# Kernel tuning notes

Hardware: AMD Instinct MI355X
Metric: run time of the kernel (lower is better)

## Reference

```python
import jax, jax.numpy as jnp
import numpy as np

NUM_TOKENS = 8192
DIM = 256
BETA = 0.25
DECAY = 0.99
EPS = 1e-05


def setup_inputs() -> dict:
    key = jax.random.key(0)
    k1, k2 = jax.random.split(key, 2)
    z = jax.random.normal(k1, (16, DIM, 32, 32), dtype=jnp.float32)
    embedding = jax.random.normal(k2, (NUM_TOKENS, DIM), dtype=jnp.float32)
    cluster_size = jnp.zeros((NUM_TOKENS,), dtype=jnp.float32)
    ema_w = embedding  # module init copies embed_init into both embedding and ema_w
    return {"z": z, "embedding": embedding, "cluster_size": cluster_size, "ema_w": ema_w}


def reference(z, embedding, cluster_size, ema_w):
    # z: [B, D, H, W] -> [B, H, W, D]
    zp = jnp.transpose(z, (0, 2, 3, 1))
    zf = zp.reshape(-1, DIM)  # [N, D]
    # squared euclidean distances [N, K] via ||z||^2 + ||e||^2 - 2 z.e
    d = (jnp.sum(zf * zf, axis=1, keepdims=True)
         + jnp.sum(embedding * embedding, axis=1)
         - 2.0 * (zf @ embedding.T))
    idx = jnp.argmin(d, axis=1)  # [N]
    z_q = embedding[idx].reshape(zp.shape)  # [B, H, W, D]

    # training-mode EMA statistics (pure-functional: returned as new states)
    counts = jax.ops.segment_sum(jnp.ones(zf.shape[0], dtype=zf.dtype), idx,
                                 num_segments=NUM_TOKENS)
    embed_sum = jax.ops.segment_sum(zf, idx, num_segments=NUM_TOKENS)  # [K, D]
    cs = cluster_size * DECAY + (1.0 - DECAY) * counts
    new_ema_w = ema_w * DECAY + (1.0 - DECAY) * embed_sum
    # torch evaluates sum AFTER add_(eps): denom = sum(cs + eps) + K*eps
    cs = cs + EPS
    new_cluster_size = cs / (jnp.sum(cs) + NUM_TOKENS * EPS)
    new_embedding = new_ema_w / new_cluster_size[:, None]

    loss = BETA * jnp.mean((jax.lax.stop_gradient(z_q) - zp) ** 2)
    # straight-through estimator
    z_q_st = zp + jax.lax.stop_gradient(z_q - zp)
    out = jnp.transpose(z_q_st, (0, 3, 1, 2))  # back to [B, D, H, W]
    return out, loss, idx, new_cluster_size, new_ema_w, new_embedding
```

## Files before the change

### kernel.cpp

```cpp
#include <hip/hip_runtime.h>

#define N_TOK   16384
#define K_CODES 8192
#define DIMS    256

#define OUT_OFF  0
#define LOSS_OFF 4194304
#define IDX_OFF  4194305
#define NCS_OFF  4210689
#define NEMA_OFF 4218881
#define NEMB_OFF 6316033

#define WS_ZFRAG  0u
#define WS_EFRAG  16777216u
#define WS_ENORM  25165824u
#define WS_PVAL   25198592u
#define WS_PIDX   25460736u
#define WS_IDXI   25722880u
#define WS_CNT    25788416u
#define WS_CS     25821184u
#define WS_OFFS   25853952u
#define WS_WPOS   25886720u
#define WS_TLIST  25919488u
#define WS_DENOM  25985024u

typedef _Float16 f16x8 __attribute__((ext_vector_type(8)));
typedef float    f32x16 __attribute__((ext_vector_type(16)));

union HU { _Float16 h; unsigned short u; };

static __device__ inline void split_f32(float x, unsigned short& hi, unsigned short& lo) {
    HU a; a.h = (_Float16)x;
    float r = (x - (float)a.h) * 2048.0f;
    HU b; b.h = (_Float16)r;
    hi = a.u; lo = b.u;
}

static __device__ inline float join_f16(unsigned short h, unsigned short l) {
    HU a, b; a.u = h; b.u = l;
    return (float)a.h + (float)b.h * 4.8828125e-4f;
}

#define GLD16(gp, lp) __builtin_amdgcn_global_load_lds( \
    (const __attribute__((address_space(1))) unsigned int*)(gp), \
    (__attribute__((address_space(3))) unsigned int*)(lp), 16, 0, 0)

__global__ __launch_bounds__(256) void cvt_z_kernel(const float* __restrict__ z,
                                                    unsigned short* __restrict__ zfrag,
                                                    float* __restrict__ loss_cell,
                                                    double* __restrict__ denom) {
    __shared__ float T[64][65];
    const int t = threadIdx.x;
    const int hg = blockIdx.x & 15, dg = (blockIdx.x >> 4) & 3, b = blockIdx.x >> 6;
    if (blockIdx.x == 0 && t == 0) { *loss_cell = 0.f; *denom = 0.0; }
    const int c4 = (t & 15) * 4, r0 = t >> 4;
    const float* zb = z + (((size_t)(b * 256 + dg * 64)) << 10) + hg * 64;
#pragma unroll
    for (int p = 0; p < 4; ++p) {
        const int r = r0 + p * 16;
        const float4 v = *(const float4*)(zb + ((size_t)r << 10) + c4);
        T[r][c4] = v.x; T[r][c4 + 1] = v.y; T[r][c4 + 2] = v.z; T[r][c4 + 3] = v.w;
    }
    __syncthreads();
    const int tr = t & 63, dc = (t >> 6) * 16;
    const int tile = b * 16 + hg;
    const int tg = tile * 2 + (tr >> 5), l31 = tr & 31;
    const int ks = dg * 4 + (dc >> 4);
    unsigned short hb[16], lb[16];
#pragma unroll
    for (int j = 0; j < 16; ++j) split_f32(T[dc + j][tr], hb[j], lb[j]);
#pragma unroll
    for (int lv = 0; lv < 2; ++lv) {
        const unsigned short* src = lv ? lb : hb;
        unsigned short* dst = zfrag + (size_t)((tg * 2 + lv) * 16 + ks) * 512;
        *(uint4*)(dst + l31 * 8)       = ((const uint4*)src)[0];
        *(uint4*)(dst + 256 + l31 * 8) = ((const uint4*)src)[1];
    }
}

__global__ __launch_bounds__(256) void cvt_e_enorm(const float* __restrict__ emb,
                                                   unsigned short* __restrict__ efrag,
                                                   float* __restrict__ enorm,
                                                   int* __restrict__ cnt) {
    __shared__ double red[256];
    const int t = threadIdx.x, g = blockIdx.x;
    const int lane = t & 63, q = t >> 6;
    const int l31 = lane & 31, lhi = lane >> 5;
    if (g < 32) cnt[g * 256 + t] = 0;
    const float* rowp = emb + (size_t)(g * 32 + l31) * 256 + lhi * 8;
    double s = 0.0;
#pragma unroll
    for (int kk = 0; kk < 4; ++kk) {
        const int ks = q * 4 + kk;
        const float4 a = *(const float4*)(rowp + ks * 16);
        const float4 bq = *(const float4*)(rowp + ks * 16 + 4);
        const float vv[8] = {a.x, a.y, a.z, a.w, bq.x, bq.y, bq.z, bq.w};
        unsigned short hb[8], lb[8];
#pragma unroll
        for (int j = 0; j < 8; ++j) {
            split_f32(vv[j], hb[j], lb[j]);
            s += (double)vv[j] * (double)vv[j];
        }
        *(uint4*)(efrag + (size_t)((g * 2 + 0) * 16 + ks) * 512 + lane * 8) = *(const uint4*)hb;
        *(uint4*)(efrag + (size_t)((g * 2 + 1) * 16 + ks) * 512 + lane * 8) = *(const uint4*)lb;
    }
    red[t] = s;
    __syncthreads();
    if (t < 32) {
        double acc = 0.0;
#pragma unroll
        for (int qq = 0; qq < 4; ++qq) acc += red[qq * 64 + t] + red[qq * 64 + 32 + t];
        enorm[g * 32 + t] = (float)acc;
    }
}

__global__ __launch_bounds__(256, 2) void argmin_mfma(
    const unsigned short* __restrict__ zfrag, const unsigned short* __restrict__ efrag,
    const float* __restrict__ enorm, float* __restrict__ pval, int* __restrict__ pidx) {
    __shared__ __align__(16) unsigned short E[2][8192];
    __shared__ float en_s[2][64];

    const int tid = threadIdx.x, lane = tid & 63, wave = tid >> 6;
    const int tile = blockIdx.x & 127, csplit = blockIdx.x >> 7;
    const int token0 = tile * 128, code0 = csplit * 2048;

    f16x8 Zr[2][16];
    {
        const unsigned short* zb = zfrag + (size_t)(tile * 4 + wave) * 16384 + lane * 8;
#pragma unroll
        for (int lv = 0; lv < 2; ++lv)
#pragma unroll
            for (int ks = 0; ks < 16; ++ks)
                Zr[lv][ks] = *(const f16x8*)(zb + (lv * 16 + ks) * 512);
    }

    const int slv = wave >> 1, scg = wave & 1;

    float bv = 3.4e38f; int bi = 0;

#pragma unroll
    for (int ksl = 0; ksl < 4; ++ksl) {
        const unsigned short* sp = efrag +
            (size_t)(((csplit * 64 + scg) * 2 + slv) * 16 + ksl) * 512 + lane * 8;
        GLD16(sp, &E[0][(wave * 4 + ksl) * 512]);
    }
    if (tid < 64) en_s[0][tid] = enorm[code0 + tid];
    __syncthreads();

    for (int ct = 0; ct < 32; ++ct) {
        f32x16 acc_h[2], acc_l[2];
#pragma unroll
        for (int cg = 0; cg < 2; ++cg)
#pragma unroll
            for (int qq = 0; qq < 16; ++qq) { acc_h[cg][qq] = 0.f; acc_l[cg][qq] = 0.f; }

#pragma unroll
        for (int kc = 0; kc < 4; ++kc) {
            const int p = (ct * 4 + kc) & 1;
            if (!(ct == 31 && kc == 3)) {
                const int nch = ct * 4 + kc + 1;
                const int nct = nch >> 2, nkc = nch & 3;
                const int g = csplit * 64 + nct * 2 + scg;
#pragma unroll
                for (int ksl = 0; ksl < 4; ++ksl) {
                    const unsigned short* sp = efrag +
                        (size_t)((g * 2 + slv) * 16 + nkc * 4 + ksl) * 512 + lane * 8;
                    GLD16(sp, &E[p ^ 1][(wave * 4 + ksl) * 512]);
                }
            }
            if (kc == 0 && ct < 31 && tid < 64)
                en_s[(ct + 1) & 1][tid] = enorm[code0 + (ct + 1) * 64 + tid];

#pragma unroll
            for (int ksl = 0; ksl < 4; ++ksl) {
                const int ks = kc * 4 + ksl;
                f16x8 ae[2][2];
#pragma unroll
                for (int lv = 0; lv < 2; ++lv)
#pragma unroll
                    for (int cg = 0; cg < 2; ++cg)
                        ae[lv][cg] = *(const f16x8*)&E[p][((lv * 2 + cg) * 4 + ksl) * 512 + lane * 8];
#pragma unroll
                for (int cg = 0; cg < 2; ++cg) {
                    acc_h[cg] = __builtin_amdgcn_mfma_f32_32x32x16_f16(ae[0][cg], Zr[0][ks], acc_h[cg], 0, 0, 0);
                    acc_l[cg] = __builtin_amdgcn_mfma_f32_32x32x16_f16(ae[0][cg], Zr[1][ks], acc_l[cg], 0, 0, 0);
                    acc_l[cg] = __builtin_amdgcn_mfma_f32_32x32x16_f16(ae[1][cg], Zr[0][ks], acc_l[cg], 0, 0, 0);
                }
            }
            if (kc == 3) {
                const int rbase = 4 * (lane >> 5);
#pragma unroll
                for (int cg = 0; cg < 2; ++cg)
#pragma unroll
                    for (int r = 0; r < 16; ++r) {
                        const int cl = cg * 32 + (r & 3) + 8 * (r >> 2) + rbase;
                        const float s = en_s[ct & 1][cl] -
                            2.0f * (acc_h[cg][r] + acc_l[cg][r] * 4.8828125e-4f);
                        const int code = code0 + ct * 64 + cl;
                        if (s < bv) { bv = s; bi = code; }
                    }
            }
            __syncthreads();
        }
    }
    {
        const float ov = __shfl_xor(bv, 32);
        const int   oi = __shfl_xor(bi, 32);
        if (ov < bv || (ov == bv && oi < bi)) { bv = ov; bi = oi; }
    }
    if (lane < 32) {
        const int n = token0 + wave * 32 + lane;
        pval[csplit * N_TOK + n] = bv;
        pidx[csplit * N_TOK + n] = bi;
    }
}

__global__ __launch_bounds__(256) void combine4_kernel(
    const float* __restrict__ pval, const int* __restrict__ pidx,
    int* __restrict__ idx_i, float* __restrict__ idx_f, int* __restrict__ cnt) {
    const int n = blockIdx.x * 256 + threadIdx.x;
    float bv = pval[n]; int bi = pidx[n];
#pragma unroll
    for (int s = 1; s < 4; ++s) {
        const float v = pval[s * N_TOK + n];
        const int i = pidx[s * N_TOK + n];
        if (v < bv || (v == bv && i < bi)) { bv = v; bi = i; }
    }
    idx_i[n] = bi;
    idx_f[n] = (float)bi;
    atomicAdd(&cnt[bi], 1);
}

__global__ __launch_bounds__(256) void scan_kernel(const int* __restrict__ cnt,
                                                   int* __restrict__ offs,
                                                   int* __restrict__ wpos) {
    __shared__ int part[256];
    const int tid = threadIdx.x;
    const int base = tid * 32;
    int loc[32];
    int s = 0;
#pragma unroll
    for (int j = 0; j < 32; ++j) { loc[j] = cnt[base + j]; s += loc[j]; }
    part[tid] = s;
    __syncthreads();
    for (int off = 1; off < 256; off <<= 1) {
        int v = 0;
        if (tid >= off) v = part[tid - off];
        __syncthreads();
        if (tid >= off) part[tid] += v;
        __syncthreads();
    }
    int run = (tid > 0) ? part[tid - 1] : 0;
#pragma unroll
    for (int j = 0; j < 32; ++j) {
        offs[base + j] = run;
        wpos[base + j] = run;
        run += loc[j];
    }
}

__global__ __launch_bounds__(256) void scatter_cs(
    const int* __restrict__ idx_i, int* __restrict__ wpos, int* __restrict__ tlist,
    const float* __restrict__ cluster_size, const int* __restrict__ cnt,
    float* __restrict__ cs, double* __restrict__ denom) {
    __shared__ double red[256];
    const int t = threadIdx.x, b = blockIdx.x;
    if (b < 64) {
        const int n = b * 256 + t;
        const int k = idx_i[n];
        tlist[atomicAdd(&wpos[k], 1)] = n;
    } else {
        const int k = (b - 64) * 256 + t;
        const float v = cluster_size[k] * 0.99f + 0.01f * (float)cnt[k] + 1e-5f;
        cs[k] = v;
        red[t] = (double)v;
        __syncthreads();
        for (int s2 = 128; s2; s2 >>= 1) {
            if (t < s2) red[t] += red[t + s2];
            __syncthreads();
        }
        if (t == 0) atomicAdd(denom, red[0]);
    }
}

__global__ __launch_bounds__(256) void nema_gather(
    const unsigned short* __restrict__ zfrag,
    const int* __restrict__ offs, const int* __restrict__ cnt, const int* __restrict__ tlist,
    const float* __restrict__ ema_w, const float* __restrict__ cs,
    const double* __restrict__ denom, float* __restrict__ ncs_out,
    float* __restrict__ nema_out, float* __restrict__ nemb_out,
    const float* __restrict__ z, const float* __restrict__ emb,
    const int* __restrict__ idx_i, float* __restrict__ out, float* __restrict__ loss_cell) {
    __shared__ float redf[256];
    const int t = threadIdx.x;
    if (blockIdx.x < 2048) {
        const int lane = t & 63, wave = t >> 6;
        const int k = blockIdx.x * 4 + wave;
        const int l31 = lane & 31, sel = lane >> 5;
        const int beg = offs[k], c = cnt[k];
        float acc[8] = {0.f, 0.f, 0.f, 0.f, 0.f, 0.f, 0.f, 0.f};
        for (int i = 0; i < c; ++i) {
            const int tok = tlist[beg + i];
            const int tg = tok >> 5, tl = tok & 31;
            const uint4 v = *(const uint4*)(zfrag +
                (size_t)((tg * 2 + sel) * 16 + (l31 >> 1)) * 512 + (l31 & 1) * 256 + tl * 8);
            uint4 o;
            o.x = __shfl_xor((int)v.x, 32); o.y = __shfl_xor((int)v.y, 32);
            o.z = __shfl_xor((int)v.z, 32); o.w = __shfl_xor((int)v.w, 32);
            if (lane < 32) {
                const unsigned short* hp = (const unsigned short*)&v;
                const unsigned short* lp = (const unsigned short*)&o;
#pragma unroll
                for (int j = 0; j < 8; ++j) acc[j] += join_f16(hp[j], lp[j]);
            }
        }
        const float dn = (float)(*denom) + (float)K_CODES * 1e-5f;
        const float ncs = cs[k] / dn;
        if (lane == 0) ncs_out[k] = ncs;
        if (lane < 32) {
            const size_t off = ((size_t)k << 8) + l31 * 8;
#pragma unroll
            for (int j = 0; j < 8; ++j) {
                const float ne = ema_w[off + j] * 0.99f + 0.01f * acc[j];
                nema_out[off + j] = ne;
                nemb_out[off + j] = ne / ncs;
            }
        }
    } else {
        const int gb = blockIdx.x - 2048;
        const int n0 = (gb >> 2) * 64;
        const int dg = (gb & 3) * 64;
        const int b = n0 >> 10, hw0 = n0 & 1023;
        const int lane = t & 63, w = t >> 6;
        const int n = n0 + lane;
        const int k = idx_i[n];
        const float* zb = z + ((size_t)b << 18) + hw0 + lane;
        float* ob = out + ((size_t)b << 18) + hw0 + lane;
        float ls = 0.f;
#pragma unroll 4
        for (int d = dg + w; d < dg + 64; d += 4) {
            const float zv = zb[(size_t)d << 10];
            const float ev = emb[((size_t)k << 8) + d];
            ob[(size_t)d << 10] = ev;
            const float df = ev - zv;
            ls += df * df;
        }
        redf[t] = ls;
        __syncthreads();
        for (int s2 = 128; s2; s2 >>= 1) {
            if (t < s2) redf[t] += redf[t + s2];
            __syncthreads();
        }
        if (t == 0) atomicAdd(loss_cell, redf[0] * (0.25f / 4194304.0f));
    }
}

extern "C" void kernel_launch(void* const* d_in, const int* in_sizes, int n_in,
                              void* d_out, int out_size, void* d_ws, size_t ws_size,
                              hipStream_t stream) {
    const float* z            = (const float*)d_in[0];
    const float* emb          = (const float*)d_in[1];
    const float* cluster_size = (const float*)d_in[2];
    const float* ema_w        = (const float*)d_in[3];
    float* out = (float*)d_out;
    char*  wsb = (char*)d_ws;

    unsigned short* zfrag = (unsigned short*)(wsb + WS_ZFRAG);
    unsigned short* efrag = (unsigned short*)(wsb + WS_EFRAG);
    float*  enorm  = (float*)(wsb + WS_ENORM);
    float*  pval   = (float*)(wsb + WS_PVAL);
    int*    pidx   = (int*)(wsb + WS_PIDX);
    int*    idx_i  = (int*)(wsb + WS_IDXI);
    int*    cnt    = (int*)(wsb + WS_CNT);
    float*  cs     = (float*)(wsb + WS_CS);
    int*    offs   = (int*)(wsb + WS_OFFS);
    int*    wpos   = (int*)(wsb + WS_WPOS);
    int*    tlist  = (int*)(wsb + WS_TLIST);
    double* denom  = (double*)(wsb + WS_DENOM);

    cvt_z_kernel<<<1024, 256, 0, stream>>>(z, zfrag, out + LOSS_OFF, denom);
    cvt_e_enorm<<<256, 256, 0, stream>>>(emb, efrag, enorm, cnt);
    argmin_mfma<<<512, 256, 0, stream>>>(zfrag, efrag, enorm, pval, pidx);
    combine4_kernel<<<N_TOK / 256, 256, 0, stream>>>(pval, pidx, idx_i,
                                                     out + IDX_OFF, cnt);
    scan_kernel<<<1, 256, 0, stream>>>(cnt, offs, wpos);
    scatter_cs<<<96, 256, 0, stream>>>(idx_i, wpos, tlist, cluster_size, cnt, cs, denom);
    nema_gather<<<3072, 256, 0, stream>>>(zfrag, offs, cnt, tlist, ema_w, cs, denom,
                                          out + NCS_OFF, out + NEMA_OFF, out + NEMB_OFF,
                                          z, emb, idx_i, out + OUT_OFF, out + LOSS_OFF);
}
```

Measured before the change: 424.6 us.

## Fuse conversion kernels, use packed atomicMin argmin, reorder MFMAs, unroll gather

Merges the z and embedding conversion kernels into one launch, selected by block index. The per-split argmin partials are replaced with a packed 64-bit (order-preserving value, index) atomicMin, which turns the combine kernel into a plain extraction. The MFMA issue order is regrouped so that consecutive MFMAs do not depend on the same accumulator, and the nema gather loop is unrolled by two to keep more loads in flight. The main savings are launch overhead and partial-buffer traffic, paid for with atomics and an extra initialisation of the atomic buffer.

```diff
diff --git a/kernel.cpp b/kernel.cpp
--- a/kernel.cpp
+++ b/kernel.cpp
@@ -14,8 +14,7 @@
 #define WS_ZFRAG  0u
 #define WS_EFRAG  16777216u
 #define WS_ENORM  25165824u
-#define WS_PVAL   25198592u
-#define WS_PIDX   25460736u
+#define WS_AMIN   25198592u
 #define WS_IDXI   25722880u
 #define WS_CNT    25788416u
 #define WS_CS     25821184u
@@ -45,78 +44,78 @@
     (const __attribute__((address_space(1))) unsigned int*)(gp), \
     (__attribute__((address_space(3))) unsigned int*)(lp), 16, 0, 0)
 
-__global__ __launch_bounds__(256) void cvt_z_kernel(const float* __restrict__ z,
-                                                    unsigned short* __restrict__ zfrag,
-                                                    float* __restrict__ loss_cell,
-                                                    double* __restrict__ denom) {
-    __shared__ float T[64][65];
+__global__ __launch_bounds__(256) void fused_cvt(
+    const float* __restrict__ z, unsigned short* __restrict__ zfrag,
+    float* __restrict__ loss_cell, double* __restrict__ denom,
+    const float* __restrict__ emb, unsigned short* __restrict__ efrag,
+    float* __restrict__ enorm, int* __restrict__ cnt,
+    unsigned long long* __restrict__ amin) {
     const int t = threadIdx.x;
-    const int hg = blockIdx.x & 15, dg = (blockIdx.x >> 4) & 3, b = blockIdx.x >> 6;
-    if (blockIdx.x == 0 && t == 0) { *loss_cell = 0.f; *denom = 0.0; }
-    const int c4 = (t & 15) * 4, r0 = t >> 4;
-    const float* zb = z + (((size_t)(b * 256 + dg * 64)) << 10) + hg * 64;
-#pragma unroll
-    for (int p = 0; p < 4; ++p) {
-        const int r = r0 + p * 16;
-        const float4 v = *(const float4*)(zb + ((size_t)r << 10) + c4);
-        T[r][c4] = v.x; T[r][c4 + 1] = v.y; T[r][c4 + 2] = v.z; T[r][c4 + 3] = v.w;
-    }
-    __syncthreads();
-    const int tr = t & 63, dc = (t >> 6) * 16;
-    const int tile = b * 16 + hg;
-    const int tg = tile * 2 + (tr >> 5), l31 = tr & 31;
-    const int ks = dg * 4 + (dc >> 4);
-    unsigned short hb[16], lb[16];
-#pragma unroll
-    for (int j = 0; j < 16; ++j) split_f32(T[dc + j][tr], hb[j], lb[j]);
-#pragma unroll
-    for (int lv = 0; lv < 2; ++lv) {
-        const unsigned short* src = lv ? lb : hb;
-        unsigned short* dst = zfrag + (size_t)((tg * 2 + lv) * 16 + ks) * 512;
-        *(uint4*)(dst + l31 * 8)       = ((const uint4*)src)[0];
-        *(uint4*)(dst + 256 + l31 * 8) = ((const uint4*)src)[1];
-    }
-}
-
-__global__ __launch_bounds__(256) void cvt_e_enorm(const float* __restrict__ emb,
-                                                   unsigned short* __restrict__ efrag,
-                                                   float* __restrict__ enorm,
-                                                   int* __restrict__ cnt) {
-    __shared__ double red[256];
-    const int t = threadIdx.x, g = blockIdx.x;
-    const int lane = t & 63, q = t >> 6;
-    const int l31 = lane & 31, lhi = lane >> 5;
-    if (g < 32) cnt[g * 256 + t] = 0;
-    const float* rowp = emb + (size_t)(g * 32 + l31) * 256 + lhi * 8;
-    double s = 0.0;
-#pragma unroll
-    for (int kk = 0; kk < 4; ++kk) {
-        const int ks = q * 4 + kk;
-        const float4 a = *(const float4*)(rowp + ks * 16);
-        const float4 bq = *(const float4*)(rowp + ks * 16 + 4);
-        const float vv[8] = {a.x, a.y, a.z, a.w, bq.x, bq.y, bq.z, bq.w};
-        unsigned short hb[8], lb[8];
-#pragma unroll
-        for (int j = 0; j < 8; ++j) {
-            split_f32(vv[j], hb[j], lb[j]);
-            s += (double)vv[j] * (double)vv[j];
-        }
-        *(uint4*)(efrag + (size_t)((g * 2 + 0) * 16 + ks) * 512 + lane * 8) = *(const uint4*)hb;
-        *(uint4*)(efrag + (size_t)((g * 2 + 1) * 16 + ks) * 512 + lane * 8) = *(const uint4*)lb;
-    }
-    red[t] = s;
-    __syncthreads();
-    if (t < 32) {
-        double acc = 0.0;
-#pragma unroll
-        for (int qq = 0; qq < 4; ++qq) acc += red[qq * 64 + t] + red[qq * 64 + 32 + t];
-        enorm[g * 32 + t] = (float)acc;
+    if (blockIdx.x < 1024) {
+        __shared__ float T[64][65];
+        const int hg = blockIdx.x & 15, dg = (blockIdx.x >> 4) & 3, b = blockIdx.x >> 6;
+        if (blockIdx.x == 0 && t == 0) { *loss_cell = 0.f; *denom = 0.0; }
+        const int c4 = (t & 15) * 4, r0 = t >> 4;
+        const float* zb = z + (((size_t)(b * 256 + dg * 64)) << 10) + hg * 64;
+#pragma unroll
+        for (int p = 0; p < 4; ++p) {
+            const int r = r0 + p * 16;
+            const float4 v = *(const float4*)(zb + ((size_t)r << 10) + c4);
+            T[r][c4] = v.x; T[r][c4 + 1] = v.y; T[r][c4 + 2] = v.z; T[r][c4 + 3] = v.w;
+        }
+        __syncthreads();
+        const int tr = t & 63, dc = (t >> 6) * 16;
+        const int tile = b * 16 + hg;
+        const int tg = tile * 2 + (tr >> 5), l31 = tr & 31;
+        const int ks = dg * 4 + (dc >> 4);
+        unsigned short hb[16], lb[16];
+#pragma unroll
+        for (int j = 0; j < 16; ++j) split_f32(T[dc + j][tr], hb[j], lb[j]);
+#pragma unroll
+        for (int lv = 0; lv < 2; ++lv) {
+            const unsigned short* src = lv ? lb : hb;
+            unsigned short* dst = zfrag + (size_t)((tg * 2 + lv) * 16 + ks) * 512;
+            *(uint4*)(dst + l31 * 8)       = ((const uint4*)src)[0];
+            *(uint4*)(dst + 256 + l31 * 8) = ((const uint4*)src)[1];
+        }
+    } else {
+        __shared__ double red[256];
+        const int g = blockIdx.x - 1024;
+        const int lane = t & 63, q = t >> 6;
+        const int l31 = lane & 31, lhi = lane >> 5;
+        if (g < 32) cnt[g * 256 + t] = 0;
+        if (g < 64) amin[g * 256 + t] = 0xFFFFFFFFFFFFFFFFull;
+        const float* rowp = emb + (size_t)(g * 32 + l31) * 256 + lhi * 8;
+        double s = 0.0;
+#pragma unroll
+        for (int kk = 0; kk < 4; ++kk) {
+            const int ks = q * 4 + kk;
+            const float4 a = *(const float4*)(rowp + ks * 16);
+            const float4 bq = *(const float4*)(rowp + ks * 16 + 4);
+            const float vv[8] = {a.x, a.y, a.z, a.w, bq.x, bq.y, bq.z, bq.w};
+            unsigned short hb[8], lb[8];
+#pragma unroll
+            for (int j = 0; j < 8; ++j) {
+                split_f32(vv[j], hb[j], lb[j]);
+                s += (double)vv[j] * (double)vv[j];
+            }
+            *(uint4*)(efrag + (size_t)((g * 2 + 0) * 16 + ks) * 512 + lane * 8) = *(const uint4*)hb;
+            *(uint4*)(efrag + (size_t)((g * 2 + 1) * 16 + ks) * 512 + lane * 8) = *(const uint4*)lb;
+        }
+        red[t] = s;
+        __syncthreads();
+        if (t < 32) {
+            double acc = 0.0;
+#pragma unroll
+            for (int qq = 0; qq < 4; ++qq) acc += red[qq * 64 + t] + red[qq * 64 + 32 + t];
+            enorm[g * 32 + t] = (float)acc;
+        }
     }
 }
 
 __global__ __launch_bounds__(256, 2) void argmin_mfma(
     const unsigned short* __restrict__ zfrag, const unsigned short* __restrict__ efrag,
-    const float* __restrict__ enorm, float* __restrict__ pval, int* __restrict__ pidx) {
+    const float* __restrict__ enorm, unsigned long long* __restrict__ amin) {
     __shared__ __align__(16) unsigned short E[2][8192];
     __shared__ float en_s[2][64];
 
@@ -181,11 +180,14 @@
                     for (int cg = 0; cg < 2; ++cg)
                         ae[lv][cg] = *(const f16x8*)&E[p][((lv * 2 + cg) * 4 + ksl) * 512 + lane * 8];
 #pragma unroll
-                for (int cg = 0; cg < 2; ++cg) {
+                for (int cg = 0; cg < 2; ++cg)
                     acc_h[cg] = __builtin_amdgcn_mfma_f32_32x32x16_f16(ae[0][cg], Zr[0][ks], acc_h[cg], 0, 0, 0);
+#pragma unroll
+                for (int cg = 0; cg < 2; ++cg)
                     acc_l[cg] = __builtin_amdgcn_mfma_f32_32x32x16_f16(ae[0][cg], Zr[1][ks], acc_l[cg], 0, 0, 0);
+#pragma unroll
+                for (int cg = 0; cg < 2; ++cg)
                     acc_l[cg] = __builtin_amdgcn_mfma_f32_32x32x16_f16(ae[1][cg], Zr[0][ks], acc_l[cg], 0, 0, 0);
-                }
             }
             if (kc == 3) {
                 const int rbase = 4 * (lane >> 5);
@@ -210,22 +212,18 @@
     }
     if (lane < 32) {
         const int n = token0 + wave * 32 + lane;
-        pval[csplit * N_TOK + n] = bv;
-        pidx[csplit * N_TOK + n] = bi;
-    }
-}
-
-__global__ __launch_bounds__(256) void combine4_kernel(
-    const float* __restrict__ pval, const int* __restrict__ pidx,
+        unsigned int u = __float_as_uint(bv);
+        u = (u & 0x80000000u) ? ~u : (u | 0x80000000u);
+        const unsigned long long pk = ((unsigned long long)u << 32) | (unsigned int)bi;
+        atomicMin(&amin[n], pk);
+    }
+}
+
+__global__ __launch_bounds__(256) void idx_cnt_kernel(
+    const unsigned long long* __restrict__ amin,
     int* __restrict__ idx_i, float* __restrict__ idx_f, int* __restrict__ cnt) {
     const int n = blockIdx.x * 256 + threadIdx.x;
-    float bv = pval[n]; int bi = pidx[n];
-#pragma unroll
-    for (int s = 1; s < 4; ++s) {
-        const float v = pval[s * N_TOK + n];
-        const int i = pidx[s * N_TOK + n];
-        if (v < bv || (v == bv && i < bi)) { bv = v; bi = i; }
-    }
+    const int bi = (int)(unsigned int)(amin[n] & 0xFFFFFFFFull);
     idx_i[n] = bi;
     idx_f[n] = (float)bi;
     atomicAdd(&cnt[bi], 1);
@@ -299,11 +297,30 @@
         const int l31 = lane & 31, sel = lane >> 5;
         const int beg = offs[k], c = cnt[k];
         float acc[8] = {0.f, 0.f, 0.f, 0.f, 0.f, 0.f, 0.f, 0.f};
-        for (int i = 0; i < c; ++i) {
+        const size_t lidx = (size_t)((l31 >> 1) + sel * 16) * 512 + (l31 & 1) * 256;
+        int i = 0;
+        for (; i + 1 < c; i += 2) {
+            const int tokA = tlist[beg + i], tokB = tlist[beg + i + 1];
+            const uint4 vA = *(const uint4*)(zfrag + (size_t)(tokA >> 5) * 16384 + lidx + (tokA & 31) * 8);
+            const uint4 vB = *(const uint4*)(zfrag + (size_t)(tokB >> 5) * 16384 + lidx + (tokB & 31) * 8);
+            uint4 oA, oB;
+            oA.x = __shfl_xor((int)vA.x, 32); oA.y = __shfl_xor((int)vA.y, 32);
+            oA.z = __shfl_xor((int)vA.z, 32); oA.w = __shfl_xor((int)vA.w, 32);
+            oB.x = __shfl_xor((int)vB.x, 32); oB.y = __shfl_xor((int)vB.y, 32);
+            oB.z = __shfl_xor((int)vB.z, 32); oB.w = __shfl_xor((int)vB.w, 32);
+            if (lane < 32) {
+                const unsigned short* hA = (const unsigned short*)&vA;
+                const unsigned short* lA = (const unsigned short*)&oA;
+                const unsigned short* hB = (const unsigned short*)&vB;
+                const unsigned short* lB = (const unsigned short*)&oB;
+#pragma unroll
+                for (int j = 0; j < 8; ++j)
+                    acc[j] += join_f16(hA[j], lA[j]) + join_f16(hB[j], lB[j]);
+            }
+        }
+        if (i < c) {
             const int tok = tlist[beg + i];
-            const int tg = tok >> 5, tl = tok & 31;
-            const uint4 v = *(const uint4*)(zfrag +
-                (size_t)((tg * 2 + sel) * 16 + (l31 >> 1)) * 512 + (l31 & 1) * 256 + tl * 8);
+            const uint4 v = *(const uint4*)(zfrag + (size_t)(tok >> 5) * 16384 + lidx + (tok & 31) * 8);
             uint4 o;
             o.x = __shfl_xor((int)v.x, 32); o.y = __shfl_xor((int)v.y, 32);
             o.z = __shfl_xor((int)v.z, 32); o.w = __shfl_xor((int)v.w, 32);
@@ -368,8 +385,7 @@
     unsigned short* zfrag = (unsigned short*)(wsb + WS_ZFRAG);
     unsigned short* efrag = (unsigned short*)(wsb + WS_EFRAG);
     float*  enorm  = (float*)(wsb + WS_ENORM);
-    float*  pval   = (float*)(wsb + WS_PVAL);
-    int*    pidx   = (int*)(wsb + WS_PIDX);
+    unsigned long long* amin = (unsigned long long*)(wsb + WS_AMIN);
     int*    idx_i  = (int*)(wsb + WS_IDXI);
     int*    cnt    = (int*)(wsb + WS_CNT);
     float*  cs     = (float*)(wsb + WS_CS);
@@ -378,11 +394,10 @@
     int*    tlist  = (int*)(wsb + WS_TLIST);
     double* denom  = (double*)(wsb + WS_DENOM);
 
-    cvt_z_kernel<<<1024, 256, 0, stream>>>(z, zfrag, out + LOSS_OFF, denom);
-    cvt_e_enorm<<<256, 256, 0, stream>>>(emb, efrag, enorm, cnt);
-    argmin_mfma<<<512, 256, 0, stream>>>(zfrag, efrag, enorm, pval, pidx);
-    combine4_kernel<<<N_TOK / 256, 256, 0, stream>>>(pval, pidx, idx_i,
-                                                     out + IDX_OFF, cnt);
+    fused_cvt<<<1280, 256, 0, stream>>>(z, zfrag, out + LOSS_OFF, denom,
+                                        emb, efrag, enorm, cnt, amin);
+    argmin_mfma<<<512, 256, 0, stream>>>(zfrag, efrag, enorm, amin);
+    idx_cnt_kernel<<<N_TOK / 256, 256, 0, stream>>>(amin, idx_i, out + IDX_OFF, cnt);
     scan_kernel<<<1, 256, 0, stream>>>(cnt, offs, wpos);
     scatter_cs<<<96, 256, 0, stream>>>(idx_i, wpos, tlist, cluster_size, cnt, cs, denom);
     nema_gather<<<3072, 256, 0, stream>>>(zfrag, offs, cnt, tlist, ema_w, cs, denom,
```

Measured after the change: 375.5 us. 1.13x faster.
